# Kernel tuning notes

Measured on AMD Instinct MI355X. Metric: run time of the kernel, lower is better.

The kernel has to match this reference:

```python
import jax, jax.numpy as jnp
import numpy as np

SIGMA = 1.0
EPS = 1e-8  # torch nn.CosineSimilarity eps


def setup_inputs() -> dict:
    key = jax.random.key(0)
    kx, ky = jax.random.split(key)
    ex = jax.random.normal(kx, (8192, 768), dtype=jnp.float32)
    ey = jax.random.normal(ky, (16384, 768), dtype=jnp.float32)
    return {"ex": ex, "ey": ey}


def _halfnormal_log_prob(v, sigma):
    # HalfNormal(sigma).log_prob(v) = 0.5*log(2/pi) - log(sigma) - v^2/(2 sigma^2)
    logc = 0.5 * jnp.log(jnp.asarray(2.0 / np.pi, v.dtype)) - jnp.log(jnp.asarray(sigma, v.dtype))
    return logc - v * v / (2.0 * sigma * sigma)


def reference(ex, ey):
    Nx, Ny = ex.shape[0], ey.shape[0]
    # cosine similarity matrix [Nx, Ny]; norms clamped like torch CosineSimilarity
    nx = jnp.maximum(jnp.linalg.norm(ex, axis=-1), EPS)  # [Nx]
    ny = jnp.maximum(jnp.linalg.norm(ey, axis=-1), EPS)  # [Ny]
    sims = jnp.einsum('nd,md->nm', ex, ey) / (nx[:, None] * ny[None, :])
    # dim = argmax([Nx, Ny]); Nx < Ny here -> reduce over axis 1 (ey side)
    dim = int(np.argmax([Nx, Ny]))
    C = sims.max(axis=dim)  # length min(Nx, Ny)
    x = 1.0 - C[:Nx]
    y = 1.0 - C[:Ny]
    lx = _halfnormal_log_prob(x, SIGMA)
    ly = _halfnormal_log_prob(y, SIGMA)
    return ((-jnp.exp(lx) * lx).sum(), (-jnp.exp(ly) * ly).sum())
```

## Files before the change

### kernel.cpp

```cpp
#include <hip/hip_runtime.h>
#include <hip/hip_bf16.h>
#include <cstdint>

#define D_DIM 768
#define BM 128
#define BN 256
#define BK 128

typedef int   intx8    __attribute__((ext_vector_type(8)));
typedef float floatx16 __attribute__((ext_vector_type(16)));

#define SCALE_ONE 0x7F7F7F7F


__device__ inline void lds_load16(const void* g, void* lds) {
  __builtin_amdgcn_global_load_lds(
      (const __attribute__((address_space(1))) unsigned int*)g,
      (__attribute__((address_space(3))) unsigned int*)lds,
      16, 0, 0);
}

__device__ inline intx8 ldfrag(const unsigned char* p, int o0, int o1) {
  intx8 r;
  *(int4*)&r       = *(const int4*)(p + o0);
  *((int4*)&r + 1) = *(const int4*)(p + o1);
  return r;
}


__global__ __launch_bounds__(256) void norm_cast_kernel(
    const float* __restrict__ EX, const float* __restrict__ EY,
    unsigned int* __restrict__ XO, unsigned int* __restrict__ YO, int Nx) {
  int row = blockIdx.x * 4 + (threadIdx.x >> 6);
  int lane = threadIdx.x & 63;
  const float* X = (row < Nx) ? EX : EY;
  unsigned int* Y = (row < Nx) ? XO : YO;
  int r = (row < Nx) ? row : (row - Nx);
  const float4* xr = (const float4*)(X + (size_t)r * D_DIM);
  float4 a = xr[lane];
  float4 b = xr[lane + 64];
  float4 c = xr[lane + 128];
  float ss = a.x*a.x + a.y*a.y + a.z*a.z + a.w*a.w
           + b.x*b.x + b.y*b.y + b.z*b.z + b.w*b.w
           + c.x*c.x + c.y*c.y + c.z*c.z + c.w*c.w;
  #pragma unroll
  for (int off = 32; off > 0; off >>= 1) ss += __shfl_xor(ss, off, 64);
  float s = 1.0f / fmaxf(sqrtf(ss), 1e-8f);
  unsigned int* yr = Y + (size_t)r * (D_DIM / 4);
  int d;
  d = __builtin_amdgcn_cvt_pk_fp8_f32(a.x * s, a.y * s, 0, false);
  d = __builtin_amdgcn_cvt_pk_fp8_f32(a.z * s, a.w * s, d, true);
  yr[lane] = (unsigned int)d;
  d = __builtin_amdgcn_cvt_pk_fp8_f32(b.x * s, b.y * s, 0, false);
  d = __builtin_amdgcn_cvt_pk_fp8_f32(b.z * s, b.w * s, d, true);
  yr[lane + 64] = (unsigned int)d;
  d = __builtin_amdgcn_cvt_pk_fp8_f32(c.x * s, c.y * s, 0, false);
  d = __builtin_amdgcn_cvt_pk_fp8_f32(c.z * s, c.w * s, d, true);
  yr[lane + 128] = (unsigned int)d;
}


__global__ __launch_bounds__(256, 2) void gemm_max_kernel(
    const unsigned char* __restrict__ A,
    const unsigned char* __restrict__ B,
    float* __restrict__ partial,
    int Nx) {
  __shared__ unsigned char As[BM * BK];
  __shared__ unsigned char Bs[BN * BK];
  __shared__ float red[2][BM];

  const int tid  = threadIdx.x;
  const int wave = tid >> 6;
  const int lane = tid & 63;
  const int wm = wave >> 1;
  const int wn = wave & 1;
  const int l31 = lane & 31;
  const int h   = lane >> 5;
  const int skey = l31 & 7;

  const int bm0 = blockIdx.x * BM;
  const int bn0 = blockIdx.y * BN;

  floatx16 acc[2][4];
  #pragma unroll
  for (int mt = 0; mt < 2; ++mt)
    #pragma unroll
    for (int nt = 0; nt < 4; ++nt)
      acc[mt][nt] = (floatx16)(0.f);

  const unsigned char* pA0 = As + (size_t)(wm * 64 + 0  + l31) * BK;
  const unsigned char* pA1 = As + (size_t)(wm * 64 + 32 + l31) * BK;
  const unsigned char* pB0 = Bs + (size_t)(wn * 128 + 0   + l31) * BK;
  const unsigned char* pB1 = Bs + (size_t)(wn * 128 + 32  + l31) * BK;
  const unsigned char* pB2 = Bs + (size_t)(wn * 128 + 64  + l31) * BK;
  const unsigned char* pB3 = Bs + (size_t)(wn * 128 + 96  + l31) * BK;

  const int srow = lane >> 3;
  const int sj = (lane & 7) ^ (srow & 7);
  const unsigned char* gA = A + (size_t)(bm0 + wave * 32 + srow) * D_DIM + sj * 16;
  const unsigned char* gB = B + (size_t)(bn0 + wave * 64 + srow) * D_DIM + sj * 16;
  unsigned char* lA0 = As + (size_t)(wave * 32) * BK;
  unsigned char* lB0 = Bs + (size_t)(wave * 64) * BK;
  const size_t g8 = (size_t)8 * D_DIM;

  for (int k0 = 0; k0 < D_DIM; k0 += BK) {
    __syncthreads();
    #pragma unroll
    for (int i = 0; i < 4; ++i)
      lds_load16(gA + k0 + i * g8, lA0 + i * 1024);
    #pragma unroll
    for (int i = 0; i < 8; ++i)
      lds_load16(gB + k0 + i * g8, lB0 + i * 1024);
    __syncthreads();

    #pragma unroll
    for (int ks = 0; ks < 2; ++ks) {
      const int c0 = ks * 4 + 2 * h;
      const int o0 = (c0 ^ skey) * 16;
      const int o1 = ((c0 + 1) ^ skey) * 16;
      intx8 a0 = ldfrag(pA0, o0, o1);
      intx8 a1 = ldfrag(pA1, o0, o1);
      intx8 b;
      b = ldfrag(pB0, o0, o1);
      acc[0][0] = __builtin_amdgcn_mfma_scale_f32_32x32x64_f8f6f4(
          a0, b, acc[0][0], 0, 0, 0, SCALE_ONE, 0, SCALE_ONE);
      acc[1][0] = __builtin_amdgcn_mfma_scale_f32_32x32x64_f8f6f4(
          a1, b, acc[1][0], 0, 0, 0, SCALE_ONE, 0, SCALE_ONE);
      b = ldfrag(pB1, o0, o1);
      acc[0][1] = __builtin_amdgcn_mfma_scale_f32_32x32x64_f8f6f4(
          a0, b, acc[0][1], 0, 0, 0, SCALE_ONE, 0, SCALE_ONE);
      acc[1][1] = __builtin_amdgcn_mfma_scale_f32_32x32x64_f8f6f4(
          a1, b, acc[1][1], 0, 0, 0, SCALE_ONE, 0, SCALE_ONE);
      b = ldfrag(pB2, o0, o1);
      acc[0][2] = __builtin_amdgcn_mfma_scale_f32_32x32x64_f8f6f4(
          a0, b, acc[0][2], 0, 0, 0, SCALE_ONE, 0, SCALE_ONE);
      acc[1][2] = __builtin_amdgcn_mfma_scale_f32_32x32x64_f8f6f4(
          a1, b, acc[1][2], 0, 0, 0, SCALE_ONE, 0, SCALE_ONE);
      b = ldfrag(pB3, o0, o1);
      acc[0][3] = __builtin_amdgcn_mfma_scale_f32_32x32x64_f8f6f4(
          a0, b, acc[0][3], 0, 0, 0, SCALE_ONE, 0, SCALE_ONE);
      acc[1][3] = __builtin_amdgcn_mfma_scale_f32_32x32x64_f8f6f4(
          a1, b, acc[1][3], 0, 0, 0, SCALE_ONE, 0, SCALE_ONE);
    }
  }

  #pragma unroll
  for (int mt = 0; mt < 2; ++mt) {
    #pragma unroll
    for (int reg = 0; reg < 16; ++reg) {
      float v = fmaxf(fmaxf(acc[mt][0][reg], acc[mt][1][reg]),
                      fmaxf(acc[mt][2][reg], acc[mt][3][reg]));
      #pragma unroll
      for (int off = 1; off < 32; off <<= 1)
        v = fmaxf(v, __shfl_xor(v, off, 64));
      if (l31 == 0) {
        int r = wm * 64 + mt * 32 + (reg & 3) + 8 * (reg >> 2) + 4 * h;
        red[wn][r] = v;
      }
    }
  }
  __syncthreads();
  if (tid < BM) {
    float m = fmaxf(red[0][tid], red[1][tid]);
    partial[(size_t)blockIdx.y * Nx + bm0 + tid] = m;
  }
}


__global__ __launch_bounds__(256) void rowmax_kernel(
    const float* __restrict__ partial, float* __restrict__ bsum, int Nx, int ncb) {
  __shared__ float sdata[4];
  int r = blockIdx.x * blockDim.x + threadIdx.x;
  float m = -1e30f;
  for (int cb = 0; cb < ncb; ++cb)
    m = fmaxf(m, partial[(size_t)cb * Nx + r]);
  float x = 1.0f - m;
  const float logc = -0.22579135264472744f;
  float l = logc - 0.5f * x * x;
  float t = -__expf(l) * l;
  #pragma unroll
  for (int off = 32; off > 0; off >>= 1) t += __shfl_xor(t, off, 64);
  int wave = threadIdx.x >> 6;
  int lane = threadIdx.x & 63;
  if (lane == 0) sdata[wave] = t;
  __syncthreads();
  if (threadIdx.x == 0)
    bsum[blockIdx.x] = sdata[0] + sdata[1] + sdata[2] + sdata[3];
}


__global__ __launch_bounds__(64) void final_kernel(
    const float* __restrict__ bsum, float* __restrict__ out, int nb) {
  int lane = threadIdx.x;
  float s = (lane < nb) ? bsum[lane] : 0.f;
  #pragma unroll
  for (int off = 32; off > 0; off >>= 1) s += __shfl_xor(s, off, 64);
  if (lane == 0) { out[0] = s; out[1] = s; }
}


extern "C" void kernel_launch(void* const* d_in, const int* in_sizes, int n_in,
                              void* d_out, int out_size, void* d_ws, size_t ws_size,
                              hipStream_t stream) {
  const float* ex = (const float*)d_in[0];
  const float* ey = (const float*)d_in[1];
  const int Nx = in_sizes[0] / D_DIM;
  const int Ny = in_sizes[1] / D_DIM;
  const int ncb = Ny / BN;

  char* ws = (char*)d_ws;
  unsigned char* exn = (unsigned char*)ws;
  unsigned char* eyn = exn + (size_t)Nx * D_DIM;
  float* partial = (float*)(ws + (size_t)(Nx + Ny) * D_DIM);
  float* bsum    = partial + (size_t)ncb * Nx;

  norm_cast_kernel<<<(Nx + Ny) / 4, 256, 0, stream>>>(
      ex, ey, (unsigned int*)exn, (unsigned int*)eyn, Nx);
  gemm_max_kernel<<<dim3(Nx / BM, Ny / BN), 256, 0, stream>>>(exn, eyn, partial, Nx);
  rowmax_kernel<<<Nx / 256, 256, 0, stream>>>(partial, bsum, Nx, ncb);
  final_kernel<<<1, 64, 0, stream>>>(bsum, (float*)d_out, Nx / 256);
}
```

Baseline: 243.6 us.

## Triple-buffer LDS pipeline with larger 256x256 tile and 8 waves

Restructures the FP8 GEMM-max kernel to use a 256x256 block tile with 512 threads and a K step of 64. A three-stage LDS ring buffer issues global-to-LDS loads two iterations ahead, using explicit vmcnt waits and a single barrier per step so memory traffic overlaps the MFMA work. MFMA issue priority is raised, and the LDS swizzle and reduction buffer are adapted to the new layout. The larger tile cuts global traffic per flop, but it raises register and LDS pressure and halves the number of blocks, which may hurt occupancy.

```diff
diff --git a/kernel.cpp b/kernel.cpp
--- a/kernel.cpp
+++ b/kernel.cpp
@@ -1,11 +1,12 @@
 #include <hip/hip_runtime.h>
-#include <hip/hip_bf16.h>
 #include <cstdint>
 
 #define D_DIM 768
-#define BM 128
+#define BM 256
 #define BN 256
-#define BK 128
+#define BK 64
+#define NT 12
+#define BUFB (BM*BK + BN*BK)
 
 typedef int   intx8    __attribute__((ext_vector_type(8)));
 typedef float floatx16 __attribute__((ext_vector_type(16)));
@@ -60,109 +61,109 @@
 }
 
 
-__global__ __launch_bounds__(256, 2) void gemm_max_kernel(
+#define STAGE(T) do {                                                          \
+    unsigned char* dst_ = &lds[(T) % 3][0];                                    \
+    const int koff_ = (T) * BK;                                                \
+    lds_load16(gA + koff_,       dst_ + wave * 2048);                          \
+    lds_load16(gA + koff_ + g16, dst_ + wave * 2048 + 1024);                   \
+    lds_load16(gB + koff_,       dst_ + BM * BK + wave * 2048);                \
+    lds_load16(gB + koff_ + g16, dst_ + BM * BK + wave * 2048 + 1024);         \
+  } while (0)
+
+#define MFMA(d, va, vb)                                                        \
+  d = __builtin_amdgcn_mfma_scale_f32_32x32x64_f8f6f4(                         \
+      va, vb, d, 0, 0, 0, SCALE_ONE, 0, SCALE_ONE)
+
+#define KITER(T, VMC, DO_STAGE) do {                                           \
+    asm volatile("s_waitcnt vmcnt(" #VMC ")" ::: "memory");                    \
+    __builtin_amdgcn_s_barrier();                                              \
+    __builtin_amdgcn_sched_barrier(0);                                         \
+    if (DO_STAGE) STAGE((T) + 2);                                              \
+    const unsigned char* buf_ = &lds[(T) % 3][0];                              \
+    intx8 a0 = ldfrag(buf_ + arow,        o0, o1);                             \
+    intx8 a1 = ldfrag(buf_ + arow + 2048, o0, o1);                             \
+    intx8 a2 = ldfrag(buf_ + arow + 4096, o0, o1);                             \
+    intx8 a3 = ldfrag(buf_ + arow + 6144, o0, o1);                             \
+    intx8 b0 = ldfrag(buf_ + brow,        o0, o1);                             \
+    intx8 b1 = ldfrag(buf_ + brow + 2048, o0, o1);                             \
+    __builtin_amdgcn_s_setprio(1);                                             \
+    MFMA(acc[0][0], a0, b0);                                                   \
+    MFMA(acc[1][0], a1, b0);                                                   \
+    MFMA(acc[2][0], a2, b0);                                                   \
+    MFMA(acc[3][0], a3, b0);                                                   \
+    MFMA(acc[0][1], a0, b1);                                                   \
+    MFMA(acc[1][1], a1, b1);                                                   \
+    MFMA(acc[2][1], a2, b1);                                                   \
+    MFMA(acc[3][1], a3, b1);                                                   \
+    __builtin_amdgcn_s_setprio(0);                                             \
+  } while (0)
+
+__global__ __launch_bounds__(512, 2) void gemm_max_kernel(
     const unsigned char* __restrict__ A,
     const unsigned char* __restrict__ B,
     float* __restrict__ partial,
     int Nx) {
-  __shared__ unsigned char As[BM * BK];
-  __shared__ unsigned char Bs[BN * BK];
-  __shared__ float red[2][BM];
+  __shared__ unsigned char lds[3][BUFB];
 
   const int tid  = threadIdx.x;
   const int wave = tid >> 6;
   const int lane = tid & 63;
-  const int wm = wave >> 1;
-  const int wn = wave & 1;
+  const int wm = wave >> 2;
+  const int wn = wave & 3;
   const int l31 = lane & 31;
   const int h   = lane >> 5;
-  const int skey = l31 & 7;
 
   const int bm0 = blockIdx.x * BM;
   const int bn0 = blockIdx.y * BN;
 
-  floatx16 acc[2][4];
-  #pragma unroll
-  for (int mt = 0; mt < 2; ++mt)
+  floatx16 acc[4][2];
+  #pragma unroll
+  for (int m = 0; m < 4; ++m)
     #pragma unroll
-    for (int nt = 0; nt < 4; ++nt)
-      acc[mt][nt] = (floatx16)(0.f);
-
-  const unsigned char* pA0 = As + (size_t)(wm * 64 + 0  + l31) * BK;
-  const unsigned char* pA1 = As + (size_t)(wm * 64 + 32 + l31) * BK;
-  const unsigned char* pB0 = Bs + (size_t)(wn * 128 + 0   + l31) * BK;
-  const unsigned char* pB1 = Bs + (size_t)(wn * 128 + 32  + l31) * BK;
-  const unsigned char* pB2 = Bs + (size_t)(wn * 128 + 64  + l31) * BK;
-  const unsigned char* pB3 = Bs + (size_t)(wn * 128 + 96  + l31) * BK;
-
-  const int srow = lane >> 3;
-  const int sj = (lane & 7) ^ (srow & 7);
+    for (int n = 0; n < 2; ++n)
+      acc[m][n] = (floatx16)(0.f);
+
+  const int akey = l31 & 3;
+  const int o0 = ((2 * h + 0) ^ akey) * 16;
+  const int o1 = ((2 * h + 1) ^ akey) * 16;
+  const int arow = (wm * 128 + l31) * 64;
+  const int brow = BM * BK + (wn * 64 + l31) * 64;
+
+  const int srow = lane >> 2;
+  const int sj = (lane & 3) ^ (srow & 3);
   const unsigned char* gA = A + (size_t)(bm0 + wave * 32 + srow) * D_DIM + sj * 16;
-  const unsigned char* gB = B + (size_t)(bn0 + wave * 64 + srow) * D_DIM + sj * 16;
-  unsigned char* lA0 = As + (size_t)(wave * 32) * BK;
-  unsigned char* lB0 = Bs + (size_t)(wave * 64) * BK;
-  const size_t g8 = (size_t)8 * D_DIM;
-
-  for (int k0 = 0; k0 < D_DIM; k0 += BK) {
-    __syncthreads();
-    #pragma unroll
-    for (int i = 0; i < 4; ++i)
-      lds_load16(gA + k0 + i * g8, lA0 + i * 1024);
-    #pragma unroll
-    for (int i = 0; i < 8; ++i)
-      lds_load16(gB + k0 + i * g8, lB0 + i * 1024);
-    __syncthreads();
-
-    #pragma unroll
-    for (int ks = 0; ks < 2; ++ks) {
-      const int c0 = ks * 4 + 2 * h;
-      const int o0 = (c0 ^ skey) * 16;
-      const int o1 = ((c0 + 1) ^ skey) * 16;
-      intx8 a0 = ldfrag(pA0, o0, o1);
-      intx8 a1 = ldfrag(pA1, o0, o1);
-      intx8 b;
-      b = ldfrag(pB0, o0, o1);
-      acc[0][0] = __builtin_amdgcn_mfma_scale_f32_32x32x64_f8f6f4(
-          a0, b, acc[0][0], 0, 0, 0, SCALE_ONE, 0, SCALE_ONE);
-      acc[1][0] = __builtin_amdgcn_mfma_scale_f32_32x32x64_f8f6f4(
-          a1, b, acc[1][0], 0, 0, 0, SCALE_ONE, 0, SCALE_ONE);
-      b = ldfrag(pB1, o0, o1);
-      acc[0][1] = __builtin_amdgcn_mfma_scale_f32_32x32x64_f8f6f4(
-          a0, b, acc[0][1], 0, 0, 0, SCALE_ONE, 0, SCALE_ONE);
-      acc[1][1] = __builtin_amdgcn_mfma_scale_f32_32x32x64_f8f6f4(
-          a1, b, acc[1][1], 0, 0, 0, SCALE_ONE, 0, SCALE_ONE);
-      b = ldfrag(pB2, o0, o1);
-      acc[0][2] = __builtin_amdgcn_mfma_scale_f32_32x32x64_f8f6f4(
-          a0, b, acc[0][2], 0, 0, 0, SCALE_ONE, 0, SCALE_ONE);
-      acc[1][2] = __builtin_amdgcn_mfma_scale_f32_32x32x64_f8f6f4(
-          a1, b, acc[1][2], 0, 0, 0, SCALE_ONE, 0, SCALE_ONE);
-      b = ldfrag(pB3, o0, o1);
-      acc[0][3] = __builtin_amdgcn_mfma_scale_f32_32x32x64_f8f6f4(
-          a0, b, acc[0][3], 0, 0, 0, SCALE_ONE, 0, SCALE_ONE);
-      acc[1][3] = __builtin_amdgcn_mfma_scale_f32_32x32x64_f8f6f4(
-          a1, b, acc[1][3], 0, 0, 0, SCALE_ONE, 0, SCALE_ONE);
-    }
-  }
-
-  #pragma unroll
-  for (int mt = 0; mt < 2; ++mt) {
+  const unsigned char* gB = B + (size_t)(bn0 + wave * 32 + srow) * D_DIM + sj * 16;
+  const size_t g16 = (size_t)16 * D_DIM;
+
+  STAGE(0);
+  STAGE(1);
+
+  KITER(0, 4, 1);  KITER(1, 4, 1);  KITER(2, 4, 1);  KITER(3, 4, 1);
+  KITER(4, 4, 1);  KITER(5, 4, 1);  KITER(6, 4, 1);  KITER(7, 4, 1);
+  KITER(8, 4, 1);  KITER(9, 4, 1);
+  KITER(10, 4, 0);
+  KITER(11, 0, 0);
+
+  float* red = (float*)&lds[0][0];
+  #pragma unroll
+  for (int m = 0; m < 4; ++m) {
     #pragma unroll
     for (int reg = 0; reg < 16; ++reg) {
-      float v = fmaxf(fmaxf(acc[mt][0][reg], acc[mt][1][reg]),
-                      fmaxf(acc[mt][2][reg], acc[mt][3][reg]));
+      float v = fmaxf(acc[m][0][reg], acc[m][1][reg]);
       #pragma unroll
       for (int off = 1; off < 32; off <<= 1)
         v = fmaxf(v, __shfl_xor(v, off, 64));
       if (l31 == 0) {
-        int r = wm * 64 + mt * 32 + (reg & 3) + 8 * (reg >> 2) + 4 * h;
-        red[wn][r] = v;
+        int r = wm * 128 + m * 32 + (reg & 3) + 8 * (reg >> 2) + 4 * h;
+        red[wn * 256 + r] = v;
       }
     }
   }
   __syncthreads();
   if (tid < BM) {
-    float m = fmaxf(red[0][tid], red[1][tid]);
-    partial[(size_t)blockIdx.y * Nx + bm0 + tid] = m;
+    float mv = fmaxf(fmaxf(red[tid], red[256 + tid]),
+                     fmaxf(red[512 + tid], red[768 + tid]));
+    partial[(size_t)blockIdx.y * Nx + bm0 + tid] = mv;
   }
 }
 
@@ -216,7 +217,7 @@
 
   norm_cast_kernel<<<(Nx + Ny) / 4, 256, 0, stream>>>(
       ex, ey, (unsigned int*)exn, (unsigned int*)eyn, Nx);
-  gemm_max_kernel<<<dim3(Nx / BM, Ny / BN), 256, 0, stream>>>(exn, eyn, partial, Nx);
+  gemm_max_kernel<<<dim3(Nx / BM, Ny / BN), 512, 0, stream>>>(exn, eyn, partial, Nx);
   rowmax_kernel<<<Nx / 256, 256, 0, stream>>>(partial, bsum, Nx, ncb);
   final_kernel<<<1, 64, 0, stream>>>(bsum, (float*)d_out, Nx / 256);
 }
```

Result: slower. 732.9 us (+200.9%).
